# Optimization experiments

Measured on AMD Instinct MI355X. Metric: run time of the kernel, lower is better.

Reference implementation:

```python
import jax, jax.numpy as jnp
import numpy as np

N_NODES = 100000
IN_DIM, HID_DIM, OUT_DIM = 512, 256, 64
N_EDGES = 3200000


def setup_inputs() -> dict:
    key = jax.random.key(0)
    k1, k2, k3, k4, k5 = jax.random.split(key, 5)
    x = jax.random.normal(k1, (N_NODES, IN_DIM), dtype=jnp.float32)
    W1 = jax.random.normal(k2, (IN_DIM, HID_DIM), dtype=jnp.float32) * (1.0 / np.sqrt(IN_DIM))
    W2 = jax.random.normal(k3, (HID_DIM, OUT_DIM), dtype=jnp.float32) * (1.0 / np.sqrt(HID_DIM))
    src = jax.random.randint(k4, (N_EDGES,), 0, N_NODES, dtype=jnp.int64)
    dst = jax.random.randint(k5, (N_EDGES,), 0, N_NODES, dtype=jnp.int64)
    edge_index = jnp.stack([src, dst], axis=0)
    return {"x": x, "W1": W1, "W2": W2, "edge_index": edge_index}


def _gcn_norm(edge_index, n):
    # add self loops, symmetric normalization deg^-1/2 A_hat deg^-1/2
    loop = jnp.arange(n, dtype=edge_index.dtype)
    src = jnp.concatenate([edge_index[0], loop])
    dst = jnp.concatenate([edge_index[1], loop])
    deg = jax.ops.segment_sum(jnp.ones_like(dst, dtype=jnp.float32), dst, num_segments=n)
    dinv = jnp.where(deg > 0, jax.lax.rsqrt(deg), 0.0)
    norm = dinv[src] * dinv[dst]  # [E + N]
    return src, dst, norm


def _gcn_layer(x, W, src, dst, norm, n):
    h = x @ W                       # dense projection [N, D_out]
    msg = h[src] * norm[:, None]    # gather + scale  [E+N, D_out]
    return jax.ops.segment_sum(msg, dst, num_segments=n)  # scatter-add [N, D_out]


def reference(x, W1, W2, edge_index):
    n = x.shape[0]
    src, dst, norm = _gcn_norm(edge_index, n)
    # dropout p=0.0 -> identity (inference reference)
    h = _gcn_layer(x, W1, src, dst, norm, n)
    h = jax.nn.relu(h)
    out = _gcn_layer(h, W2, src, dst, norm, n)
    return out
```

## Files before the change

kernel.cpp:

```cpp
#include <hip/hip_runtime.h>


typedef short s16x8 __attribute__((ext_vector_type(8)));
typedef float f32x4 __attribute__((ext_vector_type(4)));

static constexpr int IN_DIM = 512;
static constexpr int HID = 256;
static constexpr int OUTD = 64;

static constexpr int BKT_SHIFT = 8;
static constexpr int MAX_NB = 400;
static constexpr int CAP_BIN = 32;
static constexpr int EDGES_PER_BLOCK = 8192;
static constexpr int SEG_CAP = 16384;

static __device__ __forceinline__ float bf2f(unsigned short u) {
  unsigned int x = ((unsigned int)u) << 16;
  float f;
  __builtin_memcpy(&f, &x, 4);
  return f;
}
static __device__ __forceinline__ unsigned short f2bf(float f) {
  unsigned int x;
  __builtin_memcpy(&x, &f, 4);
  unsigned int r = x + 0x7fffu + ((x >> 16) & 1u);
  return (unsigned short)(r >> 16);
}
static __device__ __forceinline__ float ub(unsigned int x, int k) {
  return (float)((x >> (8 * k)) & 0xffu);
}

__global__ __launch_bounds__(256) void pack_init_kernel(
    const float* __restrict__ W1, const float* __restrict__ W2,
    short* __restrict__ Wt1, short* __restrict__ Wt2,
    unsigned* __restrict__ bucket_cursor) {
  int idx = blockIdx.x * blockDim.x + threadIdx.x;
  if (idx < IN_DIM * HID) {
    int n = idx / IN_DIM, k = idx - n * IN_DIM;
    Wt1[idx] = (short)f2bf(W1[(size_t)k * HID + n]);
  }
  if (idx < HID * OUTD) {
    int n = idx / HID, k = idx - n * HID;
    Wt2[idx] = (short)f2bf(W2[(size_t)k * OUTD + n]);
  }
  if (idx < 512) bucket_cursor[idx] = (unsigned)idx * SEG_CAP;
}

__global__ __launch_bounds__(256) void scatter_kernel(
    const int* __restrict__ src, const int* __restrict__ dst, int E,
    unsigned* __restrict__ bucket_cursor, unsigned* __restrict__ entry_buf) {
  __shared__ unsigned cnt[MAX_NB];
  __shared__ unsigned poss[MAX_NB];
  __shared__ unsigned buf[MAX_NB * CAP_BIN];
  const int tid = threadIdx.x;
  const int e0 = blockIdx.x * EDGES_PER_BLOCK;
  const int e1 = min(E, e0 + EDGES_PER_BLOCK);
  for (int i = tid; i < MAX_NB; i += 256) cnt[i] = 0;
  __syncthreads();
  for (int e = e0 + tid; e < e1; e += 256) {
    int d = dst[e];
    unsigned entry = (((unsigned)src[e]) << 8) | ((unsigned)d & 255u);
    int bkt = d >> BKT_SHIFT;
    unsigned slot = atomicAdd(&cnt[bkt], 1u);
    if (slot < CAP_BIN) {
      buf[bkt * CAP_BIN + slot] = entry;
    } else {
      unsigned pos = atomicAdd(&bucket_cursor[bkt], 1u);
      entry_buf[pos] = entry;
    }
  }
  __syncthreads();
  for (int b = tid; b < MAX_NB; b += 256) {
    unsigned c = min(cnt[b], (unsigned)CAP_BIN);
    poss[b] = c ? atomicAdd(&bucket_cursor[b], c) : 0u;
  }
  __syncthreads();
  for (int b0 = 0; b0 < MAX_NB; b0 += 8) {
    int b = b0 + (tid >> 5);
    int i = tid & 31;
    unsigned c = min(cnt[b], (unsigned)CAP_BIN);
    if ((unsigned)i < c) entry_buf[poss[b] + i] = buf[b * CAP_BIN + i];
  }
}

__global__ __launch_bounds__(256) void build_kernel(
    const unsigned* __restrict__ entry_buf,
    const unsigned* __restrict__ bucket_cursor, int Nn,
    int* __restrict__ csr_src, unsigned* __restrict__ row_start,
    unsigned* __restrict__ row_cnt, float* __restrict__ dinv) {
  __shared__ unsigned hist[256];
  __shared__ unsigned scn[256];
  const int tid = threadIdx.x;
  const int b = blockIdx.x;
  const unsigned nb0 = (unsigned)b * SEG_CAP;
  const int n_e = (int)(bucket_cursor[b] - nb0);

  hist[tid] = 0;
  __syncthreads();
  for (int i = tid; i < n_e; i += 256)
    atomicAdd(&hist[entry_buf[nb0 + i] & 255u], 1u);
  __syncthreads();

  unsigned v = hist[tid];
  scn[tid] = v;
  __syncthreads();
  for (int off = 1; off < 256; off <<= 1) {
    unsigned t = (tid >= off) ? scn[tid - off] : 0u;
    __syncthreads();
    scn[tid] += t;
    __syncthreads();
  }
  unsigned excl = scn[tid] - v;
  __syncthreads();
  scn[tid] = excl;

  int node = (b << BKT_SHIFT) + tid;
  if (node < Nn) {
    dinv[node] = rsqrtf((float)v + 1.0f);
    row_start[node] = nb0 + excl;
    row_cnt[node] = v;
  }
  hist[tid] = 0;
  __syncthreads();

  for (int i = tid; i < n_e; i += 256) {
    unsigned en = entry_buf[nb0 + i];
    unsigned d = en & 255u;
    unsigned r = atomicAdd(&hist[d], 1u);
    csr_src[nb0 + scn[d] + r] = (int)(en >> 8);
  }
}

__global__ __launch_bounds__(512) void gemm1_kernel(
    const float* __restrict__ A, const short* __restrict__ Bt,
    unsigned char* __restrict__ q, float* __restrict__ qscale,
    const float* __restrict__ dinv, int M) {
  constexpr int K = IN_DIM;
  constexpr int BN = HID;
  constexpr int BM = 128, BK = 32;
  __shared__ short sA[BM * BK];
  __shared__ short sB[BN * BK];
  __shared__ int rmax[BM];
  const int tid = threadIdx.x;
  const int wave = tid >> 6, lane = tid & 63;
  const int lm = lane & 15, lq = lane >> 4;
  const int row0 = blockIdx.x * BM;
  const int wm0 = (wave >> 2) * 64;
  const int wn0 = (wave & 3) * 64;

  f32x4 acc[4][4];
#pragma unroll
  for (int i = 0; i < 4; i++)
#pragma unroll
    for (int j = 0; j < 4; j++) acc[i][j] = f32x4{0.f, 0.f, 0.f, 0.f};

  for (int k0 = 0; k0 < K; k0 += BK) {
    {
      int m = tid >> 2, kc = tid & 3;
      int row = row0 + m;
      float4 f0 = make_float4(0, 0, 0, 0), f1 = f0;
      if (row < M) {
        const float4* pa = (const float4*)(A + (size_t)row * K + k0 + kc * 8);
        f0 = pa[0];
        f1 = pa[1];
      }
      s16x8 v;
      v[0] = (short)f2bf(f0.x); v[1] = (short)f2bf(f0.y);
      v[2] = (short)f2bf(f0.z); v[3] = (short)f2bf(f0.w);
      v[4] = (short)f2bf(f1.x); v[5] = (short)f2bf(f1.y);
      v[6] = (short)f2bf(f1.z); v[7] = (short)f2bf(f1.w);
      *(s16x8*)&sA[m * BK + kc * 8] = v;
    }
#pragma unroll
    for (int i = 0; i < 2; i++) {
      int idx = tid + i * 512;
      int n = idx >> 2, kc = idx & 3;
      *(s16x8*)&sB[n * BK + kc * 8] =
          *(const s16x8*)(Bt + (size_t)n * K + k0 + kc * 8);
    }
    __syncthreads();

    s16x8 af[4], bfr[4];
#pragma unroll
    for (int mi = 0; mi < 4; mi++)
      af[mi] = *(const s16x8*)&sA[(wm0 + mi * 16 + lm) * BK + lq * 8];
#pragma unroll
    for (int ni = 0; ni < 4; ni++)
      bfr[ni] = *(const s16x8*)&sB[(wn0 + ni * 16 + lm) * BK + lq * 8];
#pragma unroll
    for (int mi = 0; mi < 4; mi++)
#pragma unroll
      for (int ni = 0; ni < 4; ni++)
        acc[mi][ni] = __builtin_amdgcn_mfma_f32_16x16x32_bf16(
            af[mi], bfr[ni], acc[mi][ni], 0, 0, 0);
    __syncthreads();
  }

  for (int i = tid; i < BM; i += 512) rmax[i] = 0;
  __syncthreads();
#pragma unroll
  for (int mi = 0; mi < 4; mi++)
#pragma unroll
    for (int r = 0; r < 4; r++) {
      int lrow = wm0 + mi * 16 + lq * 4 + r;
      int row = row0 + lrow;
      float di = (row < M) ? dinv[row] : 0.f;
      float mx = 0.f;
#pragma unroll
      for (int ni = 0; ni < 4; ni++) mx = fmaxf(mx, fabsf(acc[mi][ni][r]));
      mx *= di;
#pragma unroll
      for (int w = 1; w < 16; w <<= 1) mx = fmaxf(mx, __shfl_xor(mx, w));
      if (lm == 0) atomicMax(&rmax[lrow], __float_as_int(mx));
    }
  __syncthreads();
#pragma unroll
  for (int mi = 0; mi < 4; mi++)
#pragma unroll
    for (int r = 0; r < 4; r++) {
      int lrow = wm0 + mi * 16 + lq * 4 + r;
      int row = row0 + lrow;
      if (row >= M) continue;
      float di = dinv[row];
      float rm = __int_as_float(rmax[lrow]);
      float inv = 127.0f / fmaxf(rm, 1e-30f);
#pragma unroll
      for (int ni = 0; ni < 4; ni++) {
        int col = wn0 + ni * 16 + lm;
        int qv = (int)rintf(acc[mi][ni][r] * di * inv) + 128;
        q[(size_t)row * BN + col] = (unsigned char)qv;
      }
      if (wn0 == 0 && lm == 0) qscale[row] = rm * (1.0f / 127.0f);
    }
}

__global__ __launch_bounds__(256) void gemm2_kernel(
    const short* __restrict__ A, const short* __restrict__ Bt,
    unsigned char* __restrict__ q, float* __restrict__ qscale,
    const float* __restrict__ dinv, int M) {
  constexpr int K = HID;
  constexpr int BN = OUTD;
  constexpr int BM = 256, BK = 32;
  __shared__ short sA[BM * BK];
  __shared__ short sB[BN * BK];
  const int tid = threadIdx.x;
  const int wave = tid >> 6, lane = tid & 63;
  const int lm = lane & 15, lq = lane >> 4;
  const int row0 = blockIdx.x * BM;
  const int wm0 = wave * 64;

  f32x4 acc[4][4];
#pragma unroll
  for (int i = 0; i < 4; i++)
#pragma unroll
    for (int j = 0; j < 4; j++) acc[i][j] = f32x4{0.f, 0.f, 0.f, 0.f};

  for (int k0 = 0; k0 < K; k0 += BK) {
#pragma unroll
    for (int i = 0; i < 4; i++) {
      int idx = tid + i * 256;
      int m = idx >> 2, kc = idx & 3;
      int row = row0 + m;
      s16x8 v = {0, 0, 0, 0, 0, 0, 0, 0};
      if (row < M) v = *(const s16x8*)(A + (size_t)row * K + k0 + kc * 8);
      *(s16x8*)&sA[m * BK + kc * 8] = v;
    }
    {
      int n = tid >> 2, kc = tid & 3;
      *(s16x8*)&sB[n * BK + kc * 8] =
          *(const s16x8*)(Bt + (size_t)n * K + k0 + kc * 8);
    }
    __syncthreads();

    s16x8 af[4], bfr[4];
#pragma unroll
    for (int mi = 0; mi < 4; mi++)
      af[mi] = *(const s16x8*)&sA[(wm0 + mi * 16 + lm) * BK + lq * 8];
#pragma unroll
    for (int ni = 0; ni < 4; ni++)
      bfr[ni] = *(const s16x8*)&sB[(ni * 16 + lm) * BK + lq * 8];
#pragma unroll
    for (int mi = 0; mi < 4; mi++)
#pragma unroll
      for (int ni = 0; ni < 4; ni++)
        acc[mi][ni] = __builtin_amdgcn_mfma_f32_16x16x32_bf16(
            af[mi], bfr[ni], acc[mi][ni], 0, 0, 0);
    __syncthreads();
  }

#pragma unroll
  for (int mi = 0; mi < 4; mi++)
#pragma unroll
    for (int r = 0; r < 4; r++) {
      int row = row0 + wm0 + mi * 16 + lq * 4 + r;
      if (row >= M) continue;
      float di = dinv[row];
      float mx = 0.f;
#pragma unroll
      for (int ni = 0; ni < 4; ni++) mx = fmaxf(mx, fabsf(acc[mi][ni][r]));
      mx *= di;
#pragma unroll
      for (int w = 1; w < 16; w <<= 1) mx = fmaxf(mx, __shfl_xor(mx, w));
      float inv = 127.0f / fmaxf(mx, 1e-30f);
#pragma unroll
      for (int ni = 0; ni < 4; ni++) {
        int col = ni * 16 + lm;
        int qv = (int)rintf(acc[mi][ni][r] * di * inv) + 128;
        q[(size_t)row * BN + col] = (unsigned char)qv;
      }
      if (lm == 0) qscale[row] = mx * (1.0f / 127.0f);
    }
}

__global__ __launch_bounds__(256) void agg1_kernel(
    const unsigned char* __restrict__ q1, const float* __restrict__ qs,
    const float* __restrict__ dinv,
    const unsigned* __restrict__ row_start, const unsigned* __restrict__ row_cnt,
    const int* __restrict__ csr_src, short* __restrict__ out, int n) {
  int node = blockIdx.x * 4 + (threadIdx.x >> 6);
  if (node >= n) return;
  const int lane = threadIdx.x & 63;
  const int half = lane >> 5;
  const int d0 = (lane & 31) * 8;
  float a[8];
#pragma unroll
  for (int j = 0; j < 8; j++) a[j] = 0.f;
  float K = 0.f;
  if (half == 0) {
    uint2 v = *(const uint2*)(q1 + (size_t)node * HID + d0);
    float w = qs[node];
    K += w;
#pragma unroll
    for (int j = 0; j < 4; j++) {
      a[j] += ub(v.x, j) * w;
      a[j + 4] += ub(v.y, j) * w;
    }
  }
  unsigned e = row_start[node] + half;
  const unsigned e1 = row_start[node] + row_cnt[node];
  for (; e + 6 < e1; e += 8) {
    int s0 = csr_src[e], s1 = csr_src[e + 2];
    int s2 = csr_src[e + 4], s3 = csr_src[e + 6];
    float w0 = qs[s0], w1 = qs[s1], w2 = qs[s2], w3 = qs[s3];
    uint2 v0 = *(const uint2*)(q1 + (size_t)s0 * HID + d0);
    uint2 v1 = *(const uint2*)(q1 + (size_t)s1 * HID + d0);
    uint2 v2 = *(const uint2*)(q1 + (size_t)s2 * HID + d0);
    uint2 v3 = *(const uint2*)(q1 + (size_t)s3 * HID + d0);
    K += (w0 + w1) + (w2 + w3);
#pragma unroll
    for (int j = 0; j < 4; j++) {
      a[j] += ub(v0.x, j) * w0 + ub(v1.x, j) * w1 + ub(v2.x, j) * w2 +
              ub(v3.x, j) * w3;
      a[j + 4] += ub(v0.y, j) * w0 + ub(v1.y, j) * w1 + ub(v2.y, j) * w2 +
                  ub(v3.y, j) * w3;
    }
  }
  for (; e < e1; e += 2) {
    int s0 = csr_src[e];
    float w0 = qs[s0];
    uint2 v0 = *(const uint2*)(q1 + (size_t)s0 * HID + d0);
    K += w0;
#pragma unroll
    for (int j = 0; j < 4; j++) {
      a[j] += ub(v0.x, j) * w0;
      a[j + 4] += ub(v0.y, j) * w0;
    }
  }
#pragma unroll
  for (int j = 0; j < 8; j++) a[j] += __shfl_xor(a[j], 32);
  K += __shfl_xor(K, 32);
  if (half == 0) {
    const float di = dinv[node];
    const float bias = 128.0f * K;
    s16x8 o;
#pragma unroll
    for (int j = 0; j < 8; j++)
      o[j] = (short)f2bf(fmaxf((a[j] - bias) * di, 0.f));
    *(s16x8*)(out + (size_t)node * HID + d0) = o;
  }
}

__global__ __launch_bounds__(256) void agg2_kernel(
    const unsigned char* __restrict__ q2, const float* __restrict__ qs,
    const float* __restrict__ dinv,
    const unsigned* __restrict__ row_start, const unsigned* __restrict__ row_cnt,
    const int* __restrict__ csr_src, float* __restrict__ out, int n) {
  int node = blockIdx.x * 4 + (threadIdx.x >> 6);
  if (node >= n) return;
  const int lane = threadIdx.x & 63;
  const int q = lane >> 4;
  const int d0 = (lane & 15) * 4;
  float a[4] = {0.f, 0.f, 0.f, 0.f};
  float K = 0.f;
  if (q == 0) {
    unsigned v = *(const unsigned*)(q2 + (size_t)node * OUTD + d0);
    float w = qs[node];
    K += w;
#pragma unroll
    for (int j = 0; j < 4; j++) a[j] += ub(v, j) * w;
  }
  unsigned e = row_start[node] + q;
  const unsigned e1 = row_start[node] + row_cnt[node];
  for (; e + 12 < e1; e += 16) {
    int s0 = csr_src[e], s1 = csr_src[e + 4];
    int s2 = csr_src[e + 8], s3 = csr_src[e + 12];
    float w0 = qs[s0], w1 = qs[s1], w2 = qs[s2], w3 = qs[s3];
    unsigned v0 = *(const unsigned*)(q2 + (size_t)s0 * OUTD + d0);
    unsigned v1 = *(const unsigned*)(q2 + (size_t)s1 * OUTD + d0);
    unsigned v2 = *(const unsigned*)(q2 + (size_t)s2 * OUTD + d0);
    unsigned v3 = *(const unsigned*)(q2 + (size_t)s3 * OUTD + d0);
    K += (w0 + w1) + (w2 + w3);
#pragma unroll
    for (int j = 0; j < 4; j++)
      a[j] += (ub(v0, j) * w0 + ub(v1, j) * w1) +
              (ub(v2, j) * w2 + ub(v3, j) * w3);
  }
  for (; e < e1; e += 4) {
    int s0 = csr_src[e];
    float w0 = qs[s0];
    unsigned v0 = *(const unsigned*)(q2 + (size_t)s0 * OUTD + d0);
    K += w0;
#pragma unroll
    for (int j = 0; j < 4; j++) a[j] += ub(v0, j) * w0;
  }
#pragma unroll
  for (int j = 0; j < 4; j++) {
    a[j] += __shfl_xor(a[j], 16);
    a[j] += __shfl_xor(a[j], 32);
  }
  K += __shfl_xor(K, 16);
  K += __shfl_xor(K, 32);
  if (q == 0) {
    const float di = dinv[node];
    const float bias = 128.0f * K;
    float4 o = make_float4((a[0] - bias) * di, (a[1] - bias) * di,
                           (a[2] - bias) * di, (a[3] - bias) * di);
    *(float4*)(out + (size_t)node * OUTD + d0) = o;
  }
}


extern "C" void kernel_launch(void* const* d_in, const int* in_sizes, int n_in,
                              void* d_out, int out_size, void* d_ws,
                              size_t ws_size, hipStream_t stream) {
  const float* x = (const float*)d_in[0];
  const float* W1 = (const float*)d_in[1];
  const float* W2 = (const float*)d_in[2];
  const int* ei = (const int*)d_in[3];
  const int E = in_sizes[3] / 2;
  const int Nn = in_sizes[0] / IN_DIM;
  const int* src = ei;
  const int* dst = ei + E;
  const int NB = (Nn + 255) >> BKT_SHIFT;

  char* p = (char*)d_ws;
  auto alloc = [&](size_t bytes) {
    char* r = p;
    p += (bytes + 255) & ~(size_t)255;
    return r;
  };
  unsigned* bucket_cursor = (unsigned*)alloc(512 * 4);
  unsigned* row_start = (unsigned*)alloc((size_t)Nn * 4);
  unsigned* row_cnt = (unsigned*)alloc((size_t)Nn * 4);
  float* dinv = (float*)alloc((size_t)Nn * 4);
  float* qs1 = (float*)alloc((size_t)Nn * 4);
  float* qs2 = (float*)alloc((size_t)Nn * 4);
  int* csr_src = (int*)alloc((size_t)MAX_NB * SEG_CAP * 4);
  unsigned* entry_buf = (unsigned*)alloc((size_t)MAX_NB * SEG_CAP * 4);
  short* Wt1 = (short*)alloc((size_t)IN_DIM * HID * 2);
  short* Wt2 = (short*)alloc((size_t)HID * OUTD * 2);
  short* agg1 = (short*)alloc((size_t)Nn * HID * 2);
  unsigned char* q1 = (unsigned char*)entry_buf;
  unsigned char* q2 = (unsigned char*)entry_buf + (16u << 20);

  pack_init_kernel<<<(IN_DIM * HID + 255) / 256, 256, 0, stream>>>(
      W1, W2, Wt1, Wt2, bucket_cursor);
  scatter_kernel<<<(E + EDGES_PER_BLOCK - 1) / EDGES_PER_BLOCK, 256, 0,
                   stream>>>(src, dst, E, bucket_cursor, entry_buf);
  build_kernel<<<NB, 256, 0, stream>>>(entry_buf, bucket_cursor, Nn, csr_src,
                                       row_start, row_cnt, dinv);
  gemm1_kernel<<<(Nn + 127) / 128, 512, 0, stream>>>(x, Wt1, q1, qs1, dinv,
                                                     Nn);
  agg1_kernel<<<(Nn + 3) / 4, 256, 0, stream>>>(q1, qs1, dinv, row_start,
                                                row_cnt, csr_src, agg1, Nn);
  gemm2_kernel<<<(Nn + 255) / 256, 256, 0, stream>>>(agg1, Wt2, q2, qs2, dinv,
                                                     Nn);
  agg2_kernel<<<(Nn + 3) / 4, 256, 0, stream>>>(q2, qs2, dinv, row_start,
                                                row_cnt, csr_src,
                                                (float*)d_out, Nn);
}
```

Measured before the change: 595.3 us.

## Drop LDS staging in GEMMs, use per-wave 32-row tiles with register prefetch

```diff
diff --git a/kernel.cpp b/kernel.cpp
--- a/kernel.cpp
+++ b/kernel.cpp
@@ -10,8 +10,8 @@
 
 static constexpr int BKT_SHIFT = 8;
 static constexpr int MAX_NB = 400;
-static constexpr int CAP_BIN = 32;
-static constexpr int EDGES_PER_BLOCK = 8192;
+static constexpr int CAP_BIN = 16;
+static constexpr int EDGES_PER_BLOCK = 2048;
 static constexpr int SEG_CAP = 16384;
 
 static __device__ __forceinline__ float bf2f(unsigned short u) {
@@ -75,15 +75,15 @@
     poss[b] = c ? atomicAdd(&bucket_cursor[b], c) : 0u;
   }
   __syncthreads();
-  for (int b0 = 0; b0 < MAX_NB; b0 += 8) {
-    int b = b0 + (tid >> 5);
-    int i = tid & 31;
+  for (int b0 = 0; b0 < MAX_NB; b0 += 16) {
+    int b = b0 + (tid >> 4);
+    int i = tid & 15;
     unsigned c = min(cnt[b], (unsigned)CAP_BIN);
     if ((unsigned)i < c) entry_buf[poss[b] + i] = buf[b * CAP_BIN + i];
   }
 }
 
-__global__ __launch_bounds__(256) void build_kernel(
+__global__ __launch_bounds__(512) void build_kernel(
     const unsigned* __restrict__ entry_buf,
     const unsigned* __restrict__ bucket_cursor, int Nn,
     int* __restrict__ csr_src, unsigned* __restrict__ row_start,
@@ -95,35 +95,39 @@
   const unsigned nb0 = (unsigned)b * SEG_CAP;
   const int n_e = (int)(bucket_cursor[b] - nb0);
 
-  hist[tid] = 0;
-  __syncthreads();
-  for (int i = tid; i < n_e; i += 256)
+  if (tid < 256) hist[tid] = 0;
+  __syncthreads();
+  for (int i = tid; i < n_e; i += 512)
     atomicAdd(&hist[entry_buf[nb0 + i] & 255u], 1u);
   __syncthreads();
 
-  unsigned v = hist[tid];
-  scn[tid] = v;
+  unsigned v = (tid < 256) ? hist[tid] : 0u;
+  if (tid < 256) scn[tid] = v;
   __syncthreads();
   for (int off = 1; off < 256; off <<= 1) {
-    unsigned t = (tid >= off) ? scn[tid - off] : 0u;
+    unsigned t = (tid < 256 && tid >= off) ? scn[tid - off] : 0u;
     __syncthreads();
-    scn[tid] += t;
+    if (tid < 256) scn[tid] += t;
     __syncthreads();
   }
-  unsigned excl = scn[tid] - v;
-  __syncthreads();
-  scn[tid] = excl;
-
-  int node = (b << BKT_SHIFT) + tid;
-  if (node < Nn) {
-    dinv[node] = rsqrtf((float)v + 1.0f);
-    row_start[node] = nb0 + excl;
-    row_cnt[node] = v;
-  }
-  hist[tid] = 0;
-  __syncthreads();
-
-  for (int i = tid; i < n_e; i += 256) {
+  unsigned excl = 0;
+  if (tid < 256) {
+    excl = scn[tid] - v;
+    int node = (b << BKT_SHIFT) + tid;
+    if (node < Nn) {
+      dinv[node] = rsqrtf((float)v + 1.0f);
+      row_start[node] = nb0 + excl;
+      row_cnt[node] = v;
+    }
+  }
+  __syncthreads();
+  if (tid < 256) {
+    scn[tid] = excl;
+    hist[tid] = 0;
+  }
+  __syncthreads();
+
+  for (int i = tid; i < n_e; i += 512) {
     unsigned en = entry_buf[nb0 + i];
     unsigned d = en & 255u;
     unsigned r = atomicAdd(&hist[d], 1u);
@@ -131,106 +135,75 @@
   }
 }
 
-__global__ __launch_bounds__(512) void gemm1_kernel(
+__global__ __launch_bounds__(256) void gemm1_kernel(
     const float* __restrict__ A, const short* __restrict__ Bt,
     unsigned char* __restrict__ q, float* __restrict__ qscale,
     const float* __restrict__ dinv, int M) {
   constexpr int K = IN_DIM;
-  constexpr int BN = HID;
-  constexpr int BM = 128, BK = 32;
-  __shared__ short sA[BM * BK];
-  __shared__ short sB[BN * BK];
-  __shared__ int rmax[BM];
-  const int tid = threadIdx.x;
-  const int wave = tid >> 6, lane = tid & 63;
+  constexpr int N = HID;
+  const int lane = threadIdx.x & 63;
+  const int wid = blockIdx.x * 4 + (threadIdx.x >> 6);
+  const int r0 = wid * 32;
+  if (r0 >= M) return;
   const int lm = lane & 15, lq = lane >> 4;
-  const int row0 = blockIdx.x * BM;
-  const int wm0 = (wave >> 2) * 64;
-  const int wn0 = (wave & 3) * 64;
-
-  f32x4 acc[4][4];
-#pragma unroll
-  for (int i = 0; i < 4; i++)
-#pragma unroll
-    for (int j = 0; j < 4; j++) acc[i][j] = f32x4{0.f, 0.f, 0.f, 0.f};
-
-  for (int k0 = 0; k0 < K; k0 += BK) {
-    {
-      int m = tid >> 2, kc = tid & 3;
-      int row = row0 + m;
-      float4 f0 = make_float4(0, 0, 0, 0), f1 = f0;
-      if (row < M) {
-        const float4* pa = (const float4*)(A + (size_t)row * K + k0 + kc * 8);
-        f0 = pa[0];
-        f1 = pa[1];
+
+  f32x4 acc[2][16];
+#pragma unroll
+  for (int mi = 0; mi < 2; mi++)
+#pragma unroll
+    for (int ni = 0; ni < 16; ni++) acc[mi][ni] = f32x4{0.f, 0.f, 0.f, 0.f};
+
+  const float* pa0 = A + (size_t)(r0 + lm) * K + lq * 8;
+  const float* pa1 = A + (size_t)(r0 + 16 + lm) * K + lq * 8;
+
+  auto ldA = [&](const float* p, int k0) -> s16x8 {
+    float4 f0 = *(const float4*)(p + k0);
+    float4 f1 = *(const float4*)(p + k0 + 4);
+    s16x8 v;
+    v[0] = (short)f2bf(f0.x); v[1] = (short)f2bf(f0.y);
+    v[2] = (short)f2bf(f0.z); v[3] = (short)f2bf(f0.w);
+    v[4] = (short)f2bf(f1.x); v[5] = (short)f2bf(f1.y);
+    v[6] = (short)f2bf(f1.z); v[7] = (short)f2bf(f1.w);
+    return v;
+  };
+
+  s16x8 af0 = ldA(pa0, 0), af1 = ldA(pa1, 0);
+  for (int k0 = 0; k0 < K; k0 += 32) {
+    s16x8 nf0, nf1;
+    if (k0 + 32 < K) {
+      nf0 = ldA(pa0, k0 + 32);
+      nf1 = ldA(pa1, k0 + 32);
+    }
+    const short* pb = Bt + (size_t)lm * K + k0 + lq * 8;
+#pragma unroll
+    for (int ni = 0; ni < 16; ni++) {
+      s16x8 b = *(const s16x8*)(pb + (size_t)ni * 16 * K);
+      acc[0][ni] = __builtin_amdgcn_mfma_f32_16x16x32_bf16(af0, b, acc[0][ni], 0, 0, 0);
+      acc[1][ni] = __builtin_amdgcn_mfma_f32_16x16x32_bf16(af1, b, acc[1][ni], 0, 0, 0);
+    }
+    af0 = nf0;
+    af1 = nf1;
+  }
+
+#pragma unroll
+  for (int mi = 0; mi < 2; mi++)
+#pragma unroll
+    for (int r = 0; r < 4; r++) {
+      int row = r0 + mi * 16 + lq * 4 + r;
+      float di = dinv[row];
+      float mx = 0.f;
+#pragma unroll
+      for (int ni = 0; ni < 16; ni++) mx = fmaxf(mx, fabsf(acc[mi][ni][r]));
+      mx *= di;
+#pragma unroll
+      for (int w = 1; w < 16; w <<= 1) mx = fmaxf(mx, __shfl_xor(mx, w));
+      float inv = 127.0f / fmaxf(mx, 1e-30f);
+#pragma unroll
+      for (int ni = 0; ni < 16; ni++) {
+        int qv = (int)rintf(acc[mi][ni][r] * di * inv) + 128;
+        q[(size_t)row * N + ni * 16 + lm] = (unsigned char)qv;
       }
-      s16x8 v;
-      v[0] = (short)f2bf(f0.x); v[1] = (short)f2bf(f0.y);
-      v[2] = (short)f2bf(f0.z); v[3] = (short)f2bf(f0.w);
-      v[4] = (short)f2bf(f1.x); v[5] = (short)f2bf(f1.y);
-      v[6] = (short)f2bf(f1.z); v[7] = (short)f2bf(f1.w);
-      *(s16x8*)&sA[m * BK + kc * 8] = v;
-    }
-#pragma unroll
-    for (int i = 0; i < 2; i++) {
-      int idx = tid + i * 512;
-      int n = idx >> 2, kc = idx & 3;
-      *(s16x8*)&sB[n * BK + kc * 8] =
-          *(const s16x8*)(Bt + (size_t)n * K + k0 + kc * 8);
-    }
-    __syncthreads();
-
-    s16x8 af[4], bfr[4];
-#pragma unroll
-    for (int mi = 0; mi < 4; mi++)
-      af[mi] = *(const s16x8*)&sA[(wm0 + mi * 16 + lm) * BK + lq * 8];
-#pragma unroll
-    for (int ni = 0; ni < 4; ni++)
-      bfr[ni] = *(const s16x8*)&sB[(wn0 + ni * 16 + lm) * BK + lq * 8];
-#pragma unroll
-    for (int mi = 0; mi < 4; mi++)
-#pragma unroll
-      for (int ni = 0; ni < 4; ni++)
-        acc[mi][ni] = __builtin_amdgcn_mfma_f32_16x16x32_bf16(
-            af[mi], bfr[ni], acc[mi][ni], 0, 0, 0);
-    __syncthreads();
-  }
-
-  for (int i = tid; i < BM; i += 512) rmax[i] = 0;
-  __syncthreads();
-#pragma unroll
-  for (int mi = 0; mi < 4; mi++)
-#pragma unroll
-    for (int r = 0; r < 4; r++) {
-      int lrow = wm0 + mi * 16 + lq * 4 + r;
-      int row = row0 + lrow;
-      float di = (row < M) ? dinv[row] : 0.f;
-      float mx = 0.f;
-#pragma unroll
-      for (int ni = 0; ni < 4; ni++) mx = fmaxf(mx, fabsf(acc[mi][ni][r]));
-      mx *= di;
-#pragma unroll
-      for (int w = 1; w < 16; w <<= 1) mx = fmaxf(mx, __shfl_xor(mx, w));
-      if (lm == 0) atomicMax(&rmax[lrow], __float_as_int(mx));
-    }
-  __syncthreads();
-#pragma unroll
-  for (int mi = 0; mi < 4; mi++)
-#pragma unroll
-    for (int r = 0; r < 4; r++) {
-      int lrow = wm0 + mi * 16 + lq * 4 + r;
-      int row = row0 + lrow;
-      if (row >= M) continue;
-      float di = dinv[row];
-      float rm = __int_as_float(rmax[lrow]);
-      float inv = 127.0f / fmaxf(rm, 1e-30f);
-#pragma unroll
-      for (int ni = 0; ni < 4; ni++) {
-        int col = wn0 + ni * 16 + lm;
-        int qv = (int)rintf(acc[mi][ni][r] * di * inv) + 128;
-        q[(size_t)row * BN + col] = (unsigned char)qv;
-      }
-      if (wn0 == 0 && lm == 0) qscale[row] = rm * (1.0f / 127.0f);
+      if (lm == 0) qscale[row] = mx * (1.0f / 127.0f);
     }
 }
 
@@ -239,61 +212,45 @@
     unsigned char* __restrict__ q, float* __restrict__ qscale,
     const float* __restrict__ dinv, int M) {
   constexpr int K = HID;
-  constexpr int BN = OUTD;
-  constexpr int BM = 256, BK = 32;
-  __shared__ short sA[BM * BK];
-  __shared__ short sB[BN * BK];
-  const int tid = threadIdx.x;
-  const int wave = tid >> 6, lane = tid & 63;
+  constexpr int N = OUTD;
+  const int lane = threadIdx.x & 63;
+  const int wid = blockIdx.x * 4 + (threadIdx.x >> 6);
+  const int r0 = wid * 32;
+  if (r0 >= M) return;
   const int lm = lane & 15, lq = lane >> 4;
-  const int row0 = blockIdx.x * BM;
-  const int wm0 = wave * 64;
-
-  f32x4 acc[4][4];
-#pragma unroll
-  for (int i = 0; i < 4; i++)
-#pragma unroll
-    for (int j = 0; j < 4; j++) acc[i][j] = f32x4{0.f, 0.f, 0.f, 0.f};
-
-  for (int k0 = 0; k0 < K; k0 += BK) {
-#pragma unroll
-    for (int i = 0; i < 4; i++) {
-      int idx = tid + i * 256;
-      int m = idx >> 2, kc = idx & 3;
-      int row = row0 + m;
-      s16x8 v = {0, 0, 0, 0, 0, 0, 0, 0};
-      if (row < M) v = *(const s16x8*)(A + (size_t)row * K + k0 + kc * 8);
-      *(s16x8*)&sA[m * BK + kc * 8] = v;
-    }
-    {
-      int n = tid >> 2, kc = tid & 3;
-      *(s16x8*)&sB[n * BK + kc * 8] =
-          *(const s16x8*)(Bt + (size_t)n * K + k0 + kc * 8);
-    }
-    __syncthreads();
-
-    s16x8 af[4], bfr[4];
-#pragma unroll
-    for (int mi = 0; mi < 4; mi++)
-      af[mi] = *(const s16x8*)&sA[(wm0 + mi * 16 + lm) * BK + lq * 8];
-#pragma unroll
-    for (int ni = 0; ni < 4; ni++)
-      bfr[ni] = *(const s16x8*)&sB[(ni * 16 + lm) * BK + lq * 8];
-#pragma unroll
-    for (int mi = 0; mi < 4; mi++)
-#pragma unroll
-      for (int ni = 0; ni < 4; ni++)
-        acc[mi][ni] = __builtin_amdgcn_mfma_f32_16x16x32_bf16(
-            af[mi], bfr[ni], acc[mi][ni], 0, 0, 0);
-    __syncthreads();
-  }
-
-#pragma unroll
-  for (int mi = 0; mi < 4; mi++)
+
+  f32x4 acc[2][4];
+#pragma unroll
+  for (int mi = 0; mi < 2; mi++)
+#pragma unroll
+    for (int ni = 0; ni < 4; ni++) acc[mi][ni] = f32x4{0.f, 0.f, 0.f, 0.f};
+
+  const short* pa0 = A + (size_t)(r0 + lm) * K + lq * 8;
+  const short* pa1 = A + (size_t)(r0 + 16 + lm) * K + lq * 8;
+
+  s16x8 af0 = *(const s16x8*)pa0, af1 = *(const s16x8*)pa1;
+  for (int k0 = 0; k0 < K; k0 += 32) {
+    s16x8 nf0, nf1;
+    if (k0 + 32 < K) {
+      nf0 = *(const s16x8*)(pa0 + k0 + 32);
+      nf1 = *(const s16x8*)(pa1 + k0 + 32);
+    }
+    const short* pb = Bt + (size_t)lm * K + k0 + lq * 8;
+#pragma unroll
+    for (int ni = 0; ni < 4; ni++) {
+      s16x8 b = *(const s16x8*)(pb + (size_t)ni * 16 * K);
+      acc[0][ni] = __builtin_amdgcn_mfma_f32_16x16x32_bf16(af0, b, acc[0][ni], 0, 0, 0);
+      acc[1][ni] = __builtin_amdgcn_mfma_f32_16x16x32_bf16(af1, b, acc[1][ni], 0, 0, 0);
+    }
+    af0 = nf0;
+    af1 = nf1;
+  }
+
+#pragma unroll
+  for (int mi = 0; mi < 2; mi++)
 #pragma unroll
     for (int r = 0; r < 4; r++) {
-      int row = row0 + wm0 + mi * 16 + lq * 4 + r;
-      if (row >= M) continue;
+      int row = r0 + mi * 16 + lq * 4 + r;
       float di = dinv[row];
       float mx = 0.f;
 #pragma unroll
@@ -304,9 +261,8 @@
       float inv = 127.0f / fmaxf(mx, 1e-30f);
 #pragma unroll
       for (int ni = 0; ni < 4; ni++) {
-        int col = ni * 16 + lm;
         int qv = (int)rintf(acc[mi][ni][r] * di * inv) + 128;
-        q[(size_t)row * BN + col] = (unsigned char)qv;
+        q[(size_t)row * N + ni * 16 + lm] = (unsigned char)qv;
       }
       if (lm == 0) qscale[row] = mx * (1.0f / 127.0f);
     }
@@ -477,14 +433,14 @@
       W1, W2, Wt1, Wt2, bucket_cursor);
   scatter_kernel<<<(E + EDGES_PER_BLOCK - 1) / EDGES_PER_BLOCK, 256, 0,
                    stream>>>(src, dst, E, bucket_cursor, entry_buf);
-  build_kernel<<<NB, 256, 0, stream>>>(entry_buf, bucket_cursor, Nn, csr_src,
+  build_kernel<<<NB, 512, 0, stream>>>(entry_buf, bucket_cursor, Nn, csr_src,
                                        row_start, row_cnt, dinv);
-  gemm1_kernel<<<(Nn + 127) / 128, 512, 0, stream>>>(x, Wt1, q1, qs1, dinv,
-                                                     Nn);
+  gemm1_kernel<<<(Nn / 32 + 3) / 4, 256, 0, stream>>>(x, Wt1, q1, qs1, dinv,
+                                                      Nn);
   agg1_kernel<<<(Nn + 3) / 4, 256, 0, stream>>>(q1, qs1, dinv, row_start,
                                                 row_cnt, csr_src, agg1, Nn);
-  gemm2_kernel<<<(Nn + 255) / 256, 256, 0, stream>>>(agg1, Wt2, q2, qs2, dinv,
-                                                     Nn);
+  gemm2_kernel<<<(Nn / 32 + 3) / 4, 256, 0, stream>>>(agg1, Wt2, q2, qs2,
+                                                      dinv, Nn);
   agg2_kernel<<<(Nn + 3) / 4, 256, 0, stream>>>(q2, qs2, dinv, row_start,
                                                 row_cnt, csr_src,
                                                 (float*)d_out, Nn);
```

Result: slower. 808.4 us (+35.8%).

## Prefetch next GEMM tiles into registers and retune edge scatter/build sizes

Applied to the files above, without the earlier changes.

```diff
diff --git a/kernel.cpp b/kernel.cpp
--- a/kernel.cpp
+++ b/kernel.cpp
@@ -10,8 +10,8 @@
 
 static constexpr int BKT_SHIFT = 8;
 static constexpr int MAX_NB = 400;
-static constexpr int CAP_BIN = 32;
-static constexpr int EDGES_PER_BLOCK = 8192;
+static constexpr int CAP_BIN = 16;
+static constexpr int EDGES_PER_BLOCK = 2048;
 static constexpr int SEG_CAP = 16384;
 
 static __device__ __forceinline__ float bf2f(unsigned short u) {
@@ -75,15 +75,15 @@
     poss[b] = c ? atomicAdd(&bucket_cursor[b], c) : 0u;
   }
   __syncthreads();
-  for (int b0 = 0; b0 < MAX_NB; b0 += 8) {
-    int b = b0 + (tid >> 5);
-    int i = tid & 31;
+  for (int b0 = 0; b0 < MAX_NB; b0 += 16) {
+    int b = b0 + (tid >> 4);
+    int i = tid & 15;
     unsigned c = min(cnt[b], (unsigned)CAP_BIN);
     if ((unsigned)i < c) entry_buf[poss[b] + i] = buf[b * CAP_BIN + i];
   }
 }
 
-__global__ __launch_bounds__(256) void build_kernel(
+__global__ __launch_bounds__(512) void build_kernel(
     const unsigned* __restrict__ entry_buf,
     const unsigned* __restrict__ bucket_cursor, int Nn,
     int* __restrict__ csr_src, unsigned* __restrict__ row_start,
@@ -95,35 +95,39 @@
   const unsigned nb0 = (unsigned)b * SEG_CAP;
   const int n_e = (int)(bucket_cursor[b] - nb0);
 
-  hist[tid] = 0;
-  __syncthreads();
-  for (int i = tid; i < n_e; i += 256)
+  if (tid < 256) hist[tid] = 0;
+  __syncthreads();
+  for (int i = tid; i < n_e; i += 512)
     atomicAdd(&hist[entry_buf[nb0 + i] & 255u], 1u);
   __syncthreads();
 
-  unsigned v = hist[tid];
-  scn[tid] = v;
+  unsigned v = (tid < 256) ? hist[tid] : 0u;
+  if (tid < 256) scn[tid] = v;
   __syncthreads();
   for (int off = 1; off < 256; off <<= 1) {
-    unsigned t = (tid >= off) ? scn[tid - off] : 0u;
+    unsigned t = (tid < 256 && tid >= off) ? scn[tid - off] : 0u;
     __syncthreads();
-    scn[tid] += t;
+    if (tid < 256) scn[tid] += t;
     __syncthreads();
   }
-  unsigned excl = scn[tid] - v;
-  __syncthreads();
-  scn[tid] = excl;
-
-  int node = (b << BKT_SHIFT) + tid;
-  if (node < Nn) {
-    dinv[node] = rsqrtf((float)v + 1.0f);
-    row_start[node] = nb0 + excl;
-    row_cnt[node] = v;
-  }
-  hist[tid] = 0;
-  __syncthreads();
-
-  for (int i = tid; i < n_e; i += 256) {
+  unsigned excl = 0;
+  if (tid < 256) {
+    excl = scn[tid] - v;
+    int node = (b << BKT_SHIFT) + tid;
+    if (node < Nn) {
+      dinv[node] = rsqrtf((float)v + 1.0f);
+      row_start[node] = nb0 + excl;
+      row_cnt[node] = v;
+    }
+  }
+  __syncthreads();
+  if (tid < 256) {
+    scn[tid] = excl;
+    hist[tid] = 0;
+  }
+  __syncthreads();
+
+  for (int i = tid; i < n_e; i += 512) {
     unsigned en = entry_buf[nb0 + i];
     unsigned d = en & 255u;
     unsigned r = atomicAdd(&hist[d], 1u);
@@ -154,29 +158,40 @@
 #pragma unroll
     for (int j = 0; j < 4; j++) acc[i][j] = f32x4{0.f, 0.f, 0.f, 0.f};
 
+  const int am = tid >> 2, akc = tid & 3;
+  const int arow = row0 + am;
+  const float* pa = A + (size_t)arow * K + akc * 8;
+  const int bn0 = tid >> 2, bkc0 = (tid & 3);
+  const int bn1 = (tid + 512) >> 2, bkc1 = (tid & 3);
+  const short* pb0 = Bt + (size_t)bn0 * K + bkc0 * 8;
+  const short* pb1 = Bt + (size_t)bn1 * K + bkc1 * 8;
+
+  float4 fa0 = make_float4(0, 0, 0, 0), fa1 = fa0;
+  if (arow < M) {
+    fa0 = *(const float4*)(pa + 0);
+    fa1 = *(const float4*)(pa + 4);
+  }
+  s16x8 vb0 = *(const s16x8*)(pb0 + 0);
+  s16x8 vb1 = *(const s16x8*)(pb1 + 0);
+
   for (int k0 = 0; k0 < K; k0 += BK) {
     {
-      int m = tid >> 2, kc = tid & 3;
-      int row = row0 + m;
-      float4 f0 = make_float4(0, 0, 0, 0), f1 = f0;
-      if (row < M) {
-        const float4* pa = (const float4*)(A + (size_t)row * K + k0 + kc * 8);
-        f0 = pa[0];
-        f1 = pa[1];
+      s16x8 v;
+      v[0] = (short)f2bf(fa0.x); v[1] = (short)f2bf(fa0.y);
+      v[2] = (short)f2bf(fa0.z); v[3] = (short)f2bf(fa0.w);
+      v[4] = (short)f2bf(fa1.x); v[5] = (short)f2bf(fa1.y);
+      v[6] = (short)f2bf(fa1.z); v[7] = (short)f2bf(fa1.w);
+      *(s16x8*)&sA[am * BK + akc * 8] = v;
+      *(s16x8*)&sB[bn0 * BK + bkc0 * 8] = vb0;
+      *(s16x8*)&sB[bn1 * BK + bkc1 * 8] = vb1;
+    }
+    if (k0 + BK < K) {
+      if (arow < M) {
+        fa0 = *(const float4*)(pa + k0 + BK);
+        fa1 = *(const float4*)(pa + k0 + BK + 4);
       }
-      s16x8 v;
-      v[0] = (short)f2bf(f0.x); v[1] = (short)f2bf(f0.y);
-      v[2] = (short)f2bf(f0.z); v[3] = (short)f2bf(f0.w);
-      v[4] = (short)f2bf(f1.x); v[5] = (short)f2bf(f1.y);
-      v[6] = (short)f2bf(f1.z); v[7] = (short)f2bf(f1.w);
-      *(s16x8*)&sA[m * BK + kc * 8] = v;
-    }
-#pragma unroll
-    for (int i = 0; i < 2; i++) {
-      int idx = tid + i * 512;
-      int n = idx >> 2, kc = idx & 3;
-      *(s16x8*)&sB[n * BK + kc * 8] =
-          *(const s16x8*)(Bt + (size_t)n * K + k0 + kc * 8);
+      vb0 = *(const s16x8*)(pb0 + k0 + BK);
+      vb1 = *(const s16x8*)(pb1 + k0 + BK);
     }
     __syncthreads();
 
@@ -255,20 +270,38 @@
 #pragma unroll
     for (int j = 0; j < 4; j++) acc[i][j] = f32x4{0.f, 0.f, 0.f, 0.f};
 
+  int amr[4];
+  const short* par[4];
+#pragma unroll
+  for (int i = 0; i < 4; i++) {
+    int idx = tid + i * 256;
+    amr[i] = idx >> 2;
+    par[i] = A + (size_t)(row0 + amr[i]) * K + (idx & 3) * 8;
+  }
+  const int bn = tid >> 2, bkc = tid & 3;
+  const short* pb = Bt + (size_t)bn * K + bkc * 8;
+
+  s16x8 va[4], vb;
+#pragma unroll
+  for (int i = 0; i < 4; i++) {
+    va[i] = s16x8{0, 0, 0, 0, 0, 0, 0, 0};
+    if (row0 + amr[i] < M) va[i] = *(const s16x8*)(par[i] + 0);
+  }
+  vb = *(const s16x8*)(pb + 0);
+
   for (int k0 = 0; k0 < K; k0 += BK) {
 #pragma unroll
     for (int i = 0; i < 4; i++) {
       int idx = tid + i * 256;
-      int m = idx >> 2, kc = idx & 3;
-      int row = row0 + m;
-      s16x8 v = {0, 0, 0, 0, 0, 0, 0, 0};
-      if (row < M) v = *(const s16x8*)(A + (size_t)row * K + k0 + kc * 8);
-      *(s16x8*)&sA[m * BK + kc * 8] = v;
-    }
-    {
-      int n = tid >> 2, kc = tid & 3;
-      *(s16x8*)&sB[n * BK + kc * 8] =
-          *(const s16x8*)(Bt + (size_t)n * K + k0 + kc * 8);
+      *(s16x8*)&sA[(idx >> 2) * BK + (idx & 3) * 8] = va[i];
+    }
+    *(s16x8*)&sB[bn * BK + bkc * 8] = vb;
+    if (k0 + BK < K) {
+#pragma unroll
+      for (int i = 0; i < 4; i++) {
+        if (row0 + amr[i] < M) va[i] = *(const s16x8*)(par[i] + k0 + BK);
+      }
+      vb = *(const s16x8*)(pb + k0 + BK);
     }
     __syncthreads();
 
@@ -477,7 +510,7 @@
       W1, W2, Wt1, Wt2, bucket_cursor);
   scatter_kernel<<<(E + EDGES_PER_BLOCK - 1) / EDGES_PER_BLOCK, 256, 0,
                    stream>>>(src, dst, E, bucket_cursor, entry_buf);
-  build_kernel<<<NB, 256, 0, stream>>>(entry_buf, bucket_cursor, Nn, csr_src,
+  build_kernel<<<NB, 512, 0, stream>>>(entry_buf, bucket_cursor, Nn, csr_src,
                                        row_start, row_cnt, dinv);
   gemm1_kernel<<<(Nn + 127) / 128, 512, 0, stream>>>(x, Wt1, q1, qs1, dinv,
                                                      Nn);
```

Result: slower. 609.8 us (+2.4%).
